# Kernel tuning notes

Measured on AMD Instinct MI355X. Metric: run time of the kernel, lower is better.

## Reference

```python
import jax, jax.numpy as jnp
import numpy as np

H = 32; W = 32; C = 128; K = 3
FS = K * K                      # filter_size = 9
CH = H - K + 1; CW = W - K + 1
F = CH * CW                     # num_convs = 900
HW = H * W                      # 1024
TEMP = 1.0                      # softmax_temp
EPS = 1e-5                      # masked_softmax epsilon
B = 8


def _build_masks():
    # local_indices[f] = flat indices of the K x K window f (row-major),
    # matching compute_input_mask with stride=1, no stochastic stride.
    idx = np.zeros((F, FS), dtype=np.int32)
    f = 0
    for i in range(CH):
        for j in range(CW):
            rows = np.arange(i, i + K)[:, None]
            cols = np.arange(j, j + K)[None, :]
            idx[f] = (rows * W + cols).reshape(-1)
            f += 1
    # global mask = (1 - local_mask) * (1 - padding_mask); padding_mask == 0 for 'valid'
    gmask = np.ones((F, HW), dtype=np.float32)
    gmask[np.arange(F)[:, None], idx] = 0.0
    return jnp.asarray(idx), jnp.asarray(gmask)


def setup_inputs() -> dict:
    key = jax.random.key(0)
    ks = jax.random.split(key, 8)
    bound = 1.0 / np.sqrt(C)  # torch nn.Linear default init
    u = lambda k, shape: jax.random.uniform(k, shape, jnp.float32, -bound, bound)
    batch = jax.random.normal(ks[0], (B, H, W, C), jnp.float32)
    Wq = u(ks[1], (C, C)); bq = u(ks[2], (C,))
    Wk = u(ks[3], (C, C)); bk = u(ks[4], (C,))
    wv = u(ks[5], (C, 1)); bv = u(ks[6], (1,))
    local_indices, gmask = _build_masks()
    return {"batch": batch, "Wq": Wq, "bq": bq, "Wk": Wk, "bk": bk,
            "wv": wv, "bv": bv, "gmask": gmask, "local_indices": local_indices}


def reference(batch, Wq, bq, Wk, bk, wv, bv, gmask, local_indices):
    # Approach '4': per-window local queries attend over global (non-window)
    # pixels; scalar values gate the local patch pixels; gated patch sums to
    # one output pixel per window. Valid padding => local pixels are unmasked
    # and the masked softmax zeroes out window/padding positions, so the
    # per-window masked linear transforms reduce exactly to full-image
    # transforms gathered/masked afterwards (no [F,B,H,W,C] materialization).
    b = batch.shape[0]
    xf = batch.reshape(b, HW, C)
    Q = xf @ Wq.T + bq                         # [B,HW,C] query_transform
    Kf = xf @ Wk.T + bk                        # [B,HW,C] key_transform
    V = (xf @ wv + bv)[..., 0]                 # [B,HW]   value_transform (C->1)
    Qg = Q[:, local_indices]                   # [B,F,FS,C] local queries (gather)
    Xl = xf[:, local_indices]                  # [B,F,FS,C] local patch features
    compat = jnp.einsum('bfpc,bqc->bfpq', Qg, Kf) / TEMP   # [B,F,FS,HW]
    # masked_softmax: exp * mask / (sum + eps), no max-subtraction (faithful)
    exps = jnp.exp(compat) * gmask[None, :, None, :]
    attn = exps / (exps.sum(-1, keepdims=True) + EPS)
    gates = jnp.einsum('bfpq,bq->bfp', attn, V)            # [B,F,FS] scalar gates
    out = jnp.einsum('bfp,bfpc->bfc', gates, Xl)           # [B,F,C]
    return out.reshape(b, CH, CW, C)
```

## Files before the change

kernel.cpp:

```cpp
#include <hip/hip_runtime.h>

#define BATCH 8
#define HW_N  1024
#define CD    128
#define W_IMG 32
#define CH_O  30
#define F_N   900

#define OFF_QH  0u
#define OFF_QL  2097152u
#define OFF_KH  4194304u
#define OFF_KL  6291456u
#define OFF_V   8388608u
#define OFF_D   8421376u
#define OFF_TP  9240576u
#define OFF_TVP 9764864u

typedef __bf16 bf16x8 __attribute__((ext_vector_type(8)));
typedef float  f32x4  __attribute__((ext_vector_type(4)));

__device__ __forceinline__ size_t frag_off(int R, int c) {
    return (size_t)(R >> 4) * 2048 +
           (size_t)((((c >> 5) * 4 + ((c >> 3) & 3)) * 128) + ((R & 15) * 8) + (c & 7));
}

__device__ __forceinline__ void async16(const __bf16* g, __bf16* l) {
    __builtin_amdgcn_global_load_lds(
        (const __attribute__((address_space(1))) unsigned int*)g,
        (__attribute__((address_space(3))) unsigned int*)l,
        16, 0, 0);
}

__global__ __launch_bounds__(256) void qkv_kernel(
    const float* __restrict__ xf,
    const float* __restrict__ Wq, const float* __restrict__ bq,
    const float* __restrict__ Wk, const float* __restrict__ bk,
    const float* __restrict__ wv, const float* __restrict__ bv,
    __bf16* __restrict__ Qh, __bf16* __restrict__ Ql,
    __bf16* __restrict__ Kh, __bf16* __restrict__ Kl,
    float* __restrict__ V)
{
    __shared__ float xs[32][132];
    __shared__ float wqs[32][132];
    __shared__ float wks[32][132];
    const int t = threadIdx.x;
    const int rowbase = blockIdx.x * 32;

#pragma unroll
    for (int m = 0; m < 4; ++m) {
        int id = t + 256 * m;
        int r  = id >> 5;
        int kq = id & 31;
        *(float4*)&xs[r][kq * 4] =
            *(const float4*)&xf[(size_t)(rowbase + r) * CD + kq * 4];
    }

    const int tx = t & 15, ty = t >> 4;

    for (int cc = 0; cc < 4; ++cc) {
        __syncthreads();
#pragma unroll
        for (int m = 0; m < 4; ++m) {
            int id = t + 256 * m;
            int r  = id >> 5;
            int kq = id & 31;
            *(float4*)&wqs[r][kq * 4] =
                *(const float4*)&Wq[(size_t)(cc * 32 + r) * CD + kq * 4];
            *(float4*)&wks[r][kq * 4] =
                *(const float4*)&Wk[(size_t)(cc * 32 + r) * CD + kq * 4];
        }
        __syncthreads();

        float aq[2][2], ak[2][2];
#pragma unroll
        for (int j = 0; j < 2; ++j)
#pragma unroll
            for (int m = 0; m < 2; ++m) { aq[j][m] = 0.f; ak[j][m] = 0.f; }

#pragma unroll 8
        for (int k = 0; k < CD; k += 4) {
            float4 x[2], q[2], kk[2];
            x[0]  = *(const float4*)&xs[ty][k];
            x[1]  = *(const float4*)&xs[ty + 16][k];
            q[0]  = *(const float4*)&wqs[tx][k];
            q[1]  = *(const float4*)&wqs[tx + 16][k];
            kk[0] = *(const float4*)&wks[tx][k];
            kk[1] = *(const float4*)&wks[tx + 16][k];
#pragma unroll
            for (int j = 0; j < 2; ++j)
#pragma unroll
                for (int m = 0; m < 2; ++m) {
                    aq[j][m] += x[j].x * q[m].x + x[j].y * q[m].y +
                                x[j].z * q[m].z + x[j].w * q[m].w;
                    ak[j][m] += x[j].x * kk[m].x + x[j].y * kk[m].y +
                                x[j].z * kk[m].z + x[j].w * kk[m].w;
                }
        }

#pragma unroll
        for (int j = 0; j < 2; ++j)
#pragma unroll
            for (int m = 0; m < 2; ++m) {
                int r = ty + 16 * j;
                int c = cc * 32 + tx + 16 * m;
                int R = rowbase + r;
                size_t o = frag_off(R, c);
                float qv = aq[j][m] + bq[c];
                float kv = ak[j][m] + bk[c];
                __bf16 qh = (__bf16)qv;
                __bf16 ql = (__bf16)(qv - (float)qh);
                __bf16 kh2 = (__bf16)kv;
                __bf16 kl2 = (__bf16)(kv - (float)kh2);
                Qh[o] = qh;  Ql[o] = ql;
                Kh[o] = kh2; Kl[o] = kl2;
            }
    }

    __syncthreads();
    if (t < 32) {
        float s = 0.f;
#pragma unroll 8
        for (int k = 0; k < CD; ++k) s += xs[t][k] * wv[k];
        V[rowbase + t] = s + bv[0];
    }
}

#define A_H 0
#define A_L 16384
#define B_H 32768
#define B_L 49152
#define VS_OFF 65536
#define ATTN_LDS_TOTAL 66048
#define SCR2 16896

__global__ __launch_bounds__(256, 2) void attn_kernel(
    const __bf16* __restrict__ Qh, const __bf16* __restrict__ Ql,
    const __bf16* __restrict__ Kh, const __bf16* __restrict__ Kl,
    const float* __restrict__ V,
    double* __restrict__ Tp, double* __restrict__ TVp,
    float* __restrict__ D)
{
    extern __shared__ char lds[];
    __bf16* Ah = (__bf16*)(lds + A_H);
    __bf16* Al = (__bf16*)(lds + A_L);
    __bf16* Bh = (__bf16*)(lds + B_H);
    __bf16* Bl = (__bf16*)(lds + B_L);
    float*  Vs = (float*)(lds + VS_OFF);

    const int b  = blockIdx.x;
    const int rb = blockIdx.y;
    const int cb = blockIdx.z;
    const int t  = threadIdx.x;
    const int w    = t >> 6;
    const int lane = t & 63;
    const int q    = lane >> 4;
    const int i    = lane & 15;
    const int wy = w >> 1, wx = w & 1;

    if (t < 128) Vs[t] = V[b * HW_N + cb * 128 + t];

    f32x4 acc[4][4];
#pragma unroll
    for (int r = 0; r < 4; ++r)
#pragma unroll
        for (int f = 0; f < 4; ++f) acc[r][f] = (f32x4){0.f, 0.f, 0.f, 0.f};

    const size_t abase = (size_t)(b * 8 + rb) * 16384;
    const size_t bbase = (size_t)(b * 8 + cb) * 16384;

    for (int kh = 0; kh < 2; ++kh) {
        __syncthreads();
#pragma unroll
        for (int m = 0; m < 4; ++m) {
            int id = t + 256 * m;
            size_t goff = (size_t)(id >> 7) * 2048 + kh * 1024 + (id & 127) * 8;
            int loff = id * 8;
            async16(Qh + abase + goff, Ah + loff);
            async16(Ql + abase + goff, Al + loff);
            async16(Kh + bbase + goff, Bh + loff);
            async16(Kl + bbase + goff, Bl + loff);
        }
        asm volatile("s_waitcnt vmcnt(0)" ::: "memory");
        __syncthreads();

#pragma unroll
        for (int kcl = 0; kcl < 2; ++kcl) {
            bf16x8 ah[4], al4[4], bh4[4], bl4[4];
#pragma unroll
            for (int r = 0; r < 4; ++r) {
                int ao = (((wy * 4 + r) * 2 + kcl) * 4 + q) * 128 + i * 8;
                ah[r]  = *(bf16x8*)&Ah[ao];
                al4[r] = *(bf16x8*)&Al[ao];
                int bo = (((wx * 4 + r) * 2 + kcl) * 4 + q) * 128 + i * 8;
                bh4[r] = *(bf16x8*)&Bh[bo];
                bl4[r] = *(bf16x8*)&Bl[bo];
            }
#pragma unroll
            for (int r = 0; r < 4; ++r)
#pragma unroll
                for (int f = 0; f < 4; ++f) {
                    acc[r][f] = __builtin_amdgcn_mfma_f32_16x16x32_bf16(
                        ah[r], bh4[f], acc[r][f], 0, 0, 0);
                    acc[r][f] = __builtin_amdgcn_mfma_f32_16x16x32_bf16(
                        ah[r], bl4[f], acc[r][f], 0, 0, 0);
                    acc[r][f] = __builtin_amdgcn_mfma_f32_16x16x32_bf16(
                        al4[r], bh4[f], acc[r][f], 0, 0, 0);
                }
        }
    }

    float st[4][4], stv[4][4];
#pragma unroll
    for (int r = 0; r < 4; ++r)
#pragma unroll
        for (int g = 0; g < 4; ++g) { st[r][g] = 0.f; stv[r][g] = 0.f; }

    const bool band = (cb - rb <= 1) && (rb - cb <= 1);

#pragma unroll
    for (int f = 0; f < 4; ++f) {
        int col_local = wx * 64 + f * 16 + i;
        int hw_c = cb * 128 + col_local;
        float v = Vs[col_local];
        int cimg_r = hw_c >> 5, cimg_c = hw_c & 31;
#pragma unroll
        for (int r = 0; r < 4; ++r)
#pragma unroll
            for (int g = 0; g < 4; ++g) {
                float e = __expf(acc[r][f][g]);
                st[r][g]  += e;
                stv[r][g] += e * v;
                if (band) {
                    int row_local = wy * 64 + r * 16 + q * 4 + g;
                    int hw_r = rb * 128 + row_local;
                    int dy = cimg_r - (hw_r >> 5);
                    int dx = cimg_c - (hw_r & 31);
                    if ((unsigned)(dy + 2) <= 4u && (unsigned)(dx + 2) <= 4u)
                        D[(size_t)(b * HW_N + hw_r) * 25 + (dy + 2) * 5 + (dx + 2)] = e;
                }
            }
    }

    __syncthreads();
    float* scrT  = (float*)lds;
    float* scrTV = (float*)(lds + SCR2);
#pragma unroll
    for (int r = 0; r < 4; ++r)
#pragma unroll
        for (int g = 0; g < 4; ++g) {
            int rl = wy * 64 + r * 16 + q * 4 + g;
            scrT [rl * 33 + wx * 16 + i] = st[r][g];
            scrTV[rl * 33 + wx * 16 + i] = stv[r][g];
        }
    __syncthreads();
    if (t < 128) {
        double s = 0.0;
#pragma unroll
        for (int c = 0; c < 32; ++c) s += (double)scrT[t * 33 + c];
        Tp[(size_t)(b * HW_N + rb * 128 + t) * 8 + cb] = s;
    } else {
        int tt = t - 128;
        double s = 0.0;
#pragma unroll
        for (int c = 0; c < 32; ++c) s += (double)scrTV[tt * 33 + c];
        TVp[(size_t)(b * HW_N + rb * 128 + tt) * 8 + cb] = s;
    }
}

__global__ __launch_bounds__(256) void gate_out_kernel(
    const float* __restrict__ xf, const float* __restrict__ V,
    const double* __restrict__ Tp, const double* __restrict__ TVp,
    const float* __restrict__ D, float* __restrict__ out)
{
    const int fi = blockIdx.x;
    const int b  = blockIdx.y;
    const int t  = threadIdx.x;

    __shared__ float  xs[96 * 128];
    __shared__ float  gates[30][9];
    __shared__ double Ts[96], TVs[96];

#pragma unroll
    for (int m = 0; m < 12; ++m) {
        int id   = t + 256 * m;
        int srow = id >> 5;
        int c4   = id & 31;
        int r3   = srow >> 5, colc = srow & 31;
        *(float4*)&xs[srow * 128 + c4 * 4] =
            *(const float4*)&xf[((size_t)(b * 32 + fi + r3) * 32 + colc) * CD + c4 * 4];
    }

    if (t < 96) {
        int R = b * HW_N + (fi + (t >> 5)) * W_IMG + (t & 31);
        double s = 0.0;
#pragma unroll
        for (int c = 0; c < 8; ++c) s += Tp[(size_t)R * 8 + c];
        Ts[t] = s;
    } else if (t >= 128 && t < 224) {
        int tt = t - 128;
        int R = b * HW_N + (fi + (tt >> 5)) * W_IMG + (tt & 31);
        double s = 0.0;
#pragma unroll
        for (int c = 0; c < 8; ++c) s += TVp[(size_t)R * 8 + c];
        TVs[tt] = s;
    }
    __syncthreads();

    for (int g = t; g < 270; g += 256) {
        int fj = g / 9, p = g % 9;
        int pr = p / 3, pc = p % 3;
        int lrow = pr * 32 + fj + pc;
        int ip = (fi + pr) * W_IMG + (fj + pc);
        const float* Drow = &D[(size_t)(b * HW_N + ip) * 25];
        double se = 0.0, sev = 0.0;
#pragma unroll
        for (int qq = 0; qq < 9; ++qq) {
            int qr = qq / 3, qc = qq % 3;
            float e = Drow[(qr - pr + 2) * 5 + (qc - pc + 2)];
            se  += (double)e;
            sev += (double)(e * V[b * HW_N + (fi + qr) * W_IMG + (fj + qc)]);
        }
        double denom = Ts[lrow] - se + 1e-5;
        double numer = TVs[lrow] - sev;
        gates[fj][p] = (float)(numer / denom);
    }
    __syncthreads();

    const int c   = t & 127;
    const int fjg = t >> 7;
#pragma unroll
    for (int it = 0; it < 15; ++it) {
        int fj = fjg * 15 + it;
        float o = 0.f;
#pragma unroll
        for (int p = 0; p < 9; ++p) {
            int pr = p / 3, pc = p % 3;
            o += gates[fj][p] * xs[(pr * 32 + fj + pc) * 128 + c];
        }
        out[((size_t)(b * F_N) + fi * CH_O + fj) * CD + c] = o;
    }
}

extern "C" void kernel_launch(void* const* d_in, const int* in_sizes, int n_in,
                              void* d_out, int out_size, void* d_ws, size_t ws_size,
                              hipStream_t stream)
{
    (void)in_sizes; (void)n_in; (void)out_size; (void)ws_size;
    const float* batch = (const float*)d_in[0];
    const float* Wq    = (const float*)d_in[1];
    const float* bq    = (const float*)d_in[2];
    const float* Wk    = (const float*)d_in[3];
    const float* bk    = (const float*)d_in[4];
    const float* wv    = (const float*)d_in[5];
    const float* bv    = (const float*)d_in[6];

    char*    ws  = (char*)d_ws;
    __bf16*  Qh  = (__bf16*)(ws + OFF_QH);
    __bf16*  Ql  = (__bf16*)(ws + OFF_QL);
    __bf16*  Kh  = (__bf16*)(ws + OFF_KH);
    __bf16*  Kl  = (__bf16*)(ws + OFF_KL);
    float*   V   = (float*)(ws + OFF_V);
    float*   D   = (float*)(ws + OFF_D);
    double*  Tp  = (double*)(ws + OFF_TP);
    double*  TVp = (double*)(ws + OFF_TVP);
    float*   out = (float*)d_out;

    qkv_kernel<<<dim3(256), dim3(256), 0, stream>>>(batch, Wq, bq, Wk, bk, wv, bv,
                                                    Qh, Ql, Kh, Kl, V);
    attn_kernel<<<dim3(8, 8, 8), dim3(256), ATTN_LDS_TOTAL, stream>>>(
        Qh, Ql, Kh, Kl, V, Tp, TVp, D);
    gate_out_kernel<<<dim3(CH_O, BATCH), dim3(256), 0, stream>>>(batch, V, Tp, TVp, D, out);
}
```

Baseline: 119.1 us.

## Compute Q/K projections with split-bf16 MFMA and pre-split weights

Replaces the scalar fp32 Q/K projection GEMM with MFMA 16x16x32 bf16 instructions, using a hi/lo split (three products) to keep roughly fp32 accuracy. A new prep kernel converts Wq/Wk once per call into hi/lo bf16 fragment layout in the workspace, and the qkv kernel now processes 16 rows per block across 512 blocks. This removes the fp32 FMA-bound projection cost but adds one extra kernel launch and reads the weight fragments directly from global memory. Precision drops slightly because the lo*lo term is omitted.

```diff
diff --git a/kernel.cpp b/kernel.cpp
--- a/kernel.cpp
+++ b/kernel.cpp
@@ -15,13 +15,18 @@
 #define OFF_D   8421376u
 #define OFF_TP  9240576u
 #define OFF_TVP 9764864u
+#define OFF_WQH 10289152u
+#define OFF_WQL 10321920u
+#define OFF_WKH 10354688u
+#define OFF_WKL 10387456u
 
 typedef __bf16 bf16x8 __attribute__((ext_vector_type(8)));
+typedef __bf16 bf16x4 __attribute__((ext_vector_type(4)));
 typedef float  f32x4  __attribute__((ext_vector_type(4)));
 
-__device__ __forceinline__ size_t frag_off(int R, int c) {
+__device__ __forceinline__ size_t frag_off(int R, int k) {
     return (size_t)(R >> 4) * 2048 +
-           (size_t)((((c >> 5) * 4 + ((c >> 3) & 3)) * 128) + ((R & 15) * 8) + (c & 7));
+           (size_t)((((k >> 5) * 4 + ((k >> 3) & 3)) * 128) + ((R & 15) * 8) + (k & 7));
 }
 
 __device__ __forceinline__ void async16(const __bf16* g, __bf16* l) {
@@ -31,93 +36,126 @@
         16, 0, 0);
 }
 
+__global__ __launch_bounds__(256) void prep_kernel(
+    const float* __restrict__ Wq, const float* __restrict__ Wk,
+    __bf16* __restrict__ WqhF, __bf16* __restrict__ WqlF,
+    __bf16* __restrict__ WkhF, __bf16* __restrict__ WklF)
+{
+    int id = blockIdx.x * 256 + threadIdx.x;
+    int c  = id >> 4;
+    int kc = id & 15;
+    size_t src = (size_t)c * CD + kc * 8;
+    size_t dst = frag_off(c, kc * 8);
+
+    float vq[8], vk[8];
+    *(float4*)&vq[0] = *(const float4*)&Wq[src];
+    *(float4*)&vq[4] = *(const float4*)&Wq[src + 4];
+    *(float4*)&vk[0] = *(const float4*)&Wk[src];
+    *(float4*)&vk[4] = *(const float4*)&Wk[src + 4];
+
+    bf16x8 qh, ql, kh, kl;
+#pragma unroll
+    for (int e = 0; e < 8; ++e) {
+        __bf16 h = (__bf16)vq[e];
+        qh[e] = h; ql[e] = (__bf16)(vq[e] - (float)h);
+        __bf16 h2 = (__bf16)vk[e];
+        kh[e] = h2; kl[e] = (__bf16)(vk[e] - (float)h2);
+    }
+    *(bf16x8*)&WqhF[dst] = qh;
+    *(bf16x8*)&WqlF[dst] = ql;
+    *(bf16x8*)&WkhF[dst] = kh;
+    *(bf16x8*)&WklF[dst] = kl;
+}
+
 __global__ __launch_bounds__(256) void qkv_kernel(
     const float* __restrict__ xf,
-    const float* __restrict__ Wq, const float* __restrict__ bq,
-    const float* __restrict__ Wk, const float* __restrict__ bk,
+    const float* __restrict__ bq, const float* __restrict__ bk,
     const float* __restrict__ wv, const float* __restrict__ bv,
+    const __bf16* __restrict__ WqhF, const __bf16* __restrict__ WqlF,
+    const __bf16* __restrict__ WkhF, const __bf16* __restrict__ WklF,
     __bf16* __restrict__ Qh, __bf16* __restrict__ Ql,
     __bf16* __restrict__ Kh, __bf16* __restrict__ Kl,
     float* __restrict__ V)
 {
-    __shared__ float xs[32][132];
-    __shared__ float wqs[32][132];
-    __shared__ float wks[32][132];
+    __shared__ float  xs[16][132];
+    __shared__ __bf16 xh[2048];
+    __shared__ __bf16 xl[2048];
+
     const int t = threadIdx.x;
-    const int rowbase = blockIdx.x * 32;
-
-#pragma unroll
-    for (int m = 0; m < 4; ++m) {
+    const int rowbase = blockIdx.x * 16;
+
+#pragma unroll
+    for (int m = 0; m < 2; ++m) {
         int id = t + 256 * m;
         int r  = id >> 5;
-        int kq = id & 31;
-        *(float4*)&xs[r][kq * 4] =
-            *(const float4*)&xf[(size_t)(rowbase + r) * CD + kq * 4];
-    }
-
-    const int tx = t & 15, ty = t >> 4;
-
-    for (int cc = 0; cc < 4; ++cc) {
-        __syncthreads();
-#pragma unroll
-        for (int m = 0; m < 4; ++m) {
-            int id = t + 256 * m;
-            int r  = id >> 5;
-            int kq = id & 31;
-            *(float4*)&wqs[r][kq * 4] =
-                *(const float4*)&Wq[(size_t)(cc * 32 + r) * CD + kq * 4];
-            *(float4*)&wks[r][kq * 4] =
-                *(const float4*)&Wk[(size_t)(cc * 32 + r) * CD + kq * 4];
-        }
-        __syncthreads();
-
-        float aq[2][2], ak[2][2];
-#pragma unroll
-        for (int j = 0; j < 2; ++j)
-#pragma unroll
-            for (int m = 0; m < 2; ++m) { aq[j][m] = 0.f; ak[j][m] = 0.f; }
-
-#pragma unroll 8
-        for (int k = 0; k < CD; k += 4) {
-            float4 x[2], q[2], kk[2];
-            x[0]  = *(const float4*)&xs[ty][k];
-            x[1]  = *(const float4*)&xs[ty + 16][k];
-            q[0]  = *(const float4*)&wqs[tx][k];
-            q[1]  = *(const float4*)&wqs[tx + 16][k];
-            kk[0] = *(const float4*)&wks[tx][k];
-            kk[1] = *(const float4*)&wks[tx + 16][k];
-#pragma unroll
-            for (int j = 0; j < 2; ++j)
-#pragma unroll
-                for (int m = 0; m < 2; ++m) {
-                    aq[j][m] += x[j].x * q[m].x + x[j].y * q[m].y +
-                                x[j].z * q[m].z + x[j].w * q[m].w;
-                    ak[j][m] += x[j].x * kk[m].x + x[j].y * kk[m].y +
-                                x[j].z * kk[m].z + x[j].w * kk[m].w;
-                }
-        }
-
-#pragma unroll
-        for (int j = 0; j < 2; ++j)
-#pragma unroll
-            for (int m = 0; m < 2; ++m) {
-                int r = ty + 16 * j;
-                int c = cc * 32 + tx + 16 * m;
-                int R = rowbase + r;
-                size_t o = frag_off(R, c);
-                float qv = aq[j][m] + bq[c];
-                float kv = ak[j][m] + bk[c];
-                __bf16 qh = (__bf16)qv;
-                __bf16 ql = (__bf16)(qv - (float)qh);
-                __bf16 kh2 = (__bf16)kv;
-                __bf16 kl2 = (__bf16)(kv - (float)kh2);
-                Qh[o] = qh;  Ql[o] = ql;
-                Kh[o] = kh2; Kl[o] = kl2;
-            }
-    }
-
+        int c4 = id & 31;
+        float4 v4 = *(const float4*)&xf[(size_t)(rowbase + r) * CD + c4 * 4];
+        *(float4*)&xs[r][c4 * 4] = v4;
+        int c = c4 * 4;
+        int off = ((c >> 5) * 4 + ((c >> 3) & 3)) * 128 + r * 8 + (c & 7);
+        float vv[4] = {v4.x, v4.y, v4.z, v4.w};
+        bf16x4 hh, ll;
+#pragma unroll
+        for (int e = 0; e < 4; ++e) {
+            __bf16 h = (__bf16)vv[e];
+            hh[e] = h; ll[e] = (__bf16)(vv[e] - (float)h);
+        }
+        *(bf16x4*)&xh[off] = hh;
+        *(bf16x4*)&xl[off] = ll;
+    }
     __syncthreads();
-    if (t < 32) {
+
+    const int w    = t >> 6;
+    const int lane = t & 63;
+    const int q    = lane >> 4;
+    const int i    = lane & 15;
+
+    f32x4 aq[2], ak[2];
+#pragma unroll
+    for (int ct = 0; ct < 2; ++ct) {
+        aq[ct] = (f32x4){0.f, 0.f, 0.f, 0.f};
+        ak[ct] = (f32x4){0.f, 0.f, 0.f, 0.f};
+    }
+
+#pragma unroll
+    for (int ks = 0; ks < 4; ++ks) {
+        const int aoff = (ks * 4 + q) * 128 + i * 8;
+        bf16x8 ah = *(bf16x8*)&xh[aoff];
+        bf16x8 al = *(bf16x8*)&xl[aoff];
+#pragma unroll
+        for (int ct = 0; ct < 2; ++ct) {
+            size_t boff = (size_t)(w * 2 + ct) * 2048 + (size_t)(ks * 4 + q) * 128 + i * 8;
+            bf16x8 bqh = *(const bf16x8*)&WqhF[boff];
+            bf16x8 bql = *(const bf16x8*)&WqlF[boff];
+            bf16x8 bkh = *(const bf16x8*)&WkhF[boff];
+            bf16x8 bkl = *(const bf16x8*)&WklF[boff];
+            aq[ct] = __builtin_amdgcn_mfma_f32_16x16x32_bf16(ah, bqh, aq[ct], 0, 0, 0);
+            aq[ct] = __builtin_amdgcn_mfma_f32_16x16x32_bf16(ah, bql, aq[ct], 0, 0, 0);
+            aq[ct] = __builtin_amdgcn_mfma_f32_16x16x32_bf16(al, bqh, aq[ct], 0, 0, 0);
+            ak[ct] = __builtin_amdgcn_mfma_f32_16x16x32_bf16(ah, bkh, ak[ct], 0, 0, 0);
+            ak[ct] = __builtin_amdgcn_mfma_f32_16x16x32_bf16(ah, bkl, ak[ct], 0, 0, 0);
+            ak[ct] = __builtin_amdgcn_mfma_f32_16x16x32_bf16(al, bkh, ak[ct], 0, 0, 0);
+        }
+    }
+
+#pragma unroll
+    for (int ct = 0; ct < 2; ++ct) {
+        int c = (w * 2 + ct) * 16 + i;
+        float bqv = bq[c], bkv = bk[c];
+#pragma unroll
+        for (int g = 0; g < 4; ++g) {
+            int R = rowbase + q * 4 + g;
+            size_t o = frag_off(R, c);
+            float qv = aq[ct][g] + bqv;
+            float kv = ak[ct][g] + bkv;
+            __bf16 h = (__bf16)qv;
+            Qh[o] = h; Ql[o] = (__bf16)(qv - (float)h);
+            __bf16 h2 = (__bf16)kv;
+            Kh[o] = h2; Kl[o] = (__bf16)(kv - (float)h2);
+        }
+    }
+
+    if (t < 16) {
         float s = 0.f;
 #pragma unroll 8
         for (int k = 0; k < CD; ++k) s += xs[t][k] * wv[k];
@@ -363,9 +401,15 @@
     float*   D   = (float*)(ws + OFF_D);
     double*  Tp  = (double*)(ws + OFF_TP);
     double*  TVp = (double*)(ws + OFF_TVP);
+    __bf16*  WqhF = (__bf16*)(ws + OFF_WQH);
+    __bf16*  WqlF = (__bf16*)(ws + OFF_WQL);
+    __bf16*  WkhF = (__bf16*)(ws + OFF_WKH);
+    __bf16*  WklF = (__bf16*)(ws + OFF_WKL);
     float*   out = (float*)d_out;
 
-    qkv_kernel<<<dim3(256), dim3(256), 0, stream>>>(batch, Wq, bq, Wk, bk, wv, bv,
+    prep_kernel<<<dim3(8), dim3(256), 0, stream>>>(Wq, Wk, WqhF, WqlF, WkhF, WklF);
+    qkv_kernel<<<dim3(512), dim3(256), 0, stream>>>(batch, bq, bk, wv, bv,
+                                                    WqhF, WqlF, WkhF, WklF,
                                                     Qh, Ql, Kh, Kl, V);
     attn_kernel<<<dim3(8, 8, 8), dim3(256), ATTN_LDS_TOTAL, stream>>>(
         Qh, Ql, Kh, Kl, V, Tp, TVp, D);
```

Measured after the change: 102.7 us. 1.16x faster.
